# Optimization experiments

Measured on AMD Instinct MI355X. Metric: run time of the kernel, lower is better.

The kernel has to match this reference:

```python
import jax, jax.numpy as jnp
import numpy as np

N, E, G = 50000, 800000, 8
IN, ED = 128, 32


def gatv2_conv(x, src, dst, ea, Wl, bl, Wr, br, We, att, bias, n_nodes):
    """PyG GATv2Conv: add self loops (edge_attr fill='mean'), per-edge GATv2
    attention with leaky_relu(0.2), softmax over incoming edges per dst,
    scatter-add of alpha * x_l[src]; concat heads + bias."""
    H, C = att.shape
    e = src.shape[0]
    # self loops: edge attr = mean of incoming edge attrs per node (0 if none)
    loop = jnp.arange(n_nodes)
    cnt = jnp.maximum(jax.ops.segment_sum(jnp.ones((e,), x.dtype), dst, n_nodes), 1.0)
    ea_loop = jax.ops.segment_sum(ea, dst, n_nodes) / cnt[:, None]
    s = jnp.concatenate([src, loop])
    d = jnp.concatenate([dst, loop])
    ea_all = jnp.concatenate([ea, ea_loop], axis=0)
    xl = (x @ Wl + bl).reshape(n_nodes, H, C)
    xr = (x @ Wr + br).reshape(n_nodes, H, C)
    ee = (ea_all @ We).reshape(-1, H, C)
    m = jax.nn.leaky_relu(xl[s] + xr[d] + ee, 0.2)          # [Etot,H,C]
    alpha = jnp.einsum('ehc,hc->eh', m, att)                 # [Etot,H]
    amax = jax.ops.segment_max(alpha, d, n_nodes)            # every node has self loop
    p = jnp.exp(alpha - amax[d])
    denom = jax.ops.segment_sum(p, d, n_nodes)
    a = p / denom[d]                                         # [Etot,H]
    out = jax.ops.segment_sum(xl[s] * a[..., None], d, n_nodes)
    return out.reshape(n_nodes, H * C) + bias


def setup_inputs() -> dict:
    key = jax.random.key(0)
    ks = jax.random.split(key, 32)
    def gl(k, shape, fan):
        return jax.random.normal(k, shape, jnp.float32) / np.sqrt(fan)
    inp = {
        'x': jax.random.normal(ks[0], (N, IN), jnp.float32),
        'edge_index': jax.random.randint(ks[1], (2, E), 0, N),
        'edge_attr': jax.random.normal(ks[2], (E, ED), jnp.float32),
        'batch': jnp.sort(jax.random.randint(ks[3], (N,), 0, G)),
        # conv1: in=128 -> heads=2, out=64
        'Wl1': gl(ks[4], (IN, 128), IN), 'bl1': jnp.zeros((128,), jnp.float32),
        'Wr1': gl(ks[5], (IN, 128), IN), 'br1': jnp.zeros((128,), jnp.float32),
        'We1': gl(ks[6], (ED, 128), ED),
        'att1': gl(ks[7], (2, 64), 64), 'bias1': jnp.zeros((128,), jnp.float32),
        # conv2: in=128 -> heads=3, out=64
        'Wl2': gl(ks[8], (128, 192), 128), 'bl2': jnp.zeros((192,), jnp.float32),
        'Wr2': gl(ks[9], (128, 192), 128), 'br2': jnp.zeros((192,), jnp.float32),
        'We2': gl(ks[10], (ED, 192), ED),
        'att2': gl(ks[11], (3, 64), 64), 'bias2': jnp.zeros((192,), jnp.float32),
        # MLP head
        'W1': gl(ks[12], (192, 64), 192), 'c1': jnp.zeros((64,), jnp.float32),
        'W2': gl(ks[13], (64, 32), 64),  'c2': jnp.zeros((32,), jnp.float32),
        'W3': gl(ks[14], (32, 16), 32),  'c3': jnp.zeros((16,), jnp.float32),
        'W4': gl(ks[15], (16, 8), 16),   'c4': jnp.zeros((8,), jnp.float32),
        'W5': gl(ks[16], (8, 1), 8),     'c5': jnp.zeros((1,), jnp.float32),
        'W6': gl(ks[17], (1, 1), 1),     'c6': jnp.zeros((1,), jnp.float32),
    }
    return inp


def reference(x, edge_index, edge_attr, batch,
              Wl1, bl1, Wr1, br1, We1, att1, bias1,
              Wl2, bl2, Wr2, br2, We2, att2, bias2,
              W1, c1, W2, c2, W3, c3, W4, c4, W5, c5, W6, c6):
    lrelu = lambda t: jax.nn.leaky_relu(t, 0.01)  # nn.LeakyReLU default slope
    src, dst = edge_index[0], edge_index[1]
    h = lrelu(gatv2_conv(x, src, dst, edge_attr, Wl1, bl1, Wr1, br1, We1, att1, bias1, N))
    h = lrelu(gatv2_conv(h, src, dst, edge_attr, Wl2, bl2, Wr2, br2, We2, att2, bias2, N))
    g = jax.ops.segment_sum(h, batch, G)           # global_add_pool -> [G,192]
    g = lrelu(g @ W1 + c1)
    g = lrelu(g @ W2 + c2)
    g = lrelu(g @ W3 + c3)
    g = lrelu(g @ W4 + c4)
    g = g @ W5 + c5
    g = g @ W6 + c6
    return g
```

## Files before the change

kernel.cpp:

```cpp
#include <hip/hip_runtime.h>
#include <hip/hip_bf16.h>
#include <math.h>


typedef __attribute__((ext_vector_type(8))) short short8v;
typedef __attribute__((ext_vector_type(4))) float f32x4;

__device__ __forceinline__ unsigned short f2bf(float f) {
    union { float f; unsigned u; } v; v.f = f;
    unsigned r = v.u + 0x7fff + ((v.u >> 16) & 1);
    return (unsigned short)(r >> 16);
}
__device__ __forceinline__ float bf2f(unsigned short b) {
    union { unsigned u; float f; } v; v.u = ((unsigned)b) << 16;
    return v.f;
}

__device__ __forceinline__ int xcd_swizzle(int bid, int nwg) {
    int sq = nwg >> 3, sr = nwg & 7;
    int xcd = bid & 7, idx = bid >> 3;
    return (xcd < sr ? xcd * (sq + 1) : sr * (sq + 1) + (xcd - sr) * sq) + idx;
}

__global__ void k_deg(const int* __restrict__ dst, int E, int* __restrict__ deg) {
    int e = blockIdx.x * blockDim.x + threadIdx.x;
    if (e < E) atomicAdd(&deg[dst[e]], 1);
}

__global__ void k_scan1(const int* __restrict__ deg, int N,
                        int* __restrict__ incl, int* __restrict__ bsum) {
    __shared__ int ws4[4];
    const int tid = threadIdx.x;
    const int lane = tid & 63, w = tid >> 6;
    const int base = blockIdx.x * 2048;
    int v[8];
    int s = 0;
#pragma unroll
    for (int j = 0; j < 8; ++j) {
        int i = base + tid * 8 + j;
        v[j] = (i < N) ? deg[i] : 0;
        s += v[j];
    }
    int ps = s;
#pragma unroll
    for (int off = 1; off < 64; off <<= 1) {
        int t = __shfl_up(ps, off);
        if (lane >= off) ps += t;
    }
    if (lane == 63) ws4[w] = ps;
    __syncthreads();
    int woffs = 0;
#pragma unroll
    for (int k = 0; k < 4; ++k)
        if (k < w) woffs += ws4[k];
    int run = ps - s + woffs;
#pragma unroll
    for (int j = 0; j < 8; ++j) {
        run += v[j];
        int i = base + tid * 8 + j;
        if (i < N) incl[i] = run;
    }
    if (tid == 255) bsum[blockIdx.x] = run;
}

__global__ void k_scan2(int* __restrict__ bsum, int nb) {
    if (threadIdx.x == 0) {
        int c = 0;
        for (int k = 0; k < nb; ++k) { int t = bsum[k]; bsum[k] = c; c += t; }
    }
}

__global__ void k_scan3(const int* __restrict__ incl, const int* __restrict__ deg,
                        const int* __restrict__ boff, int N,
                        int* __restrict__ row_ptr, int* __restrict__ woff) {
    int i = blockIdx.x * blockDim.x + threadIdx.x;
    if (i < N) {
        int v = incl[i] + boff[i >> 11];
        row_ptr[i + 1] = v;
        woff[i] = v - deg[i];
        if (i == 0) row_ptr[0] = 0;
    }
}

__global__ void k_scatter(const int* __restrict__ src, const int* __restrict__ dst,
                          int E, int* __restrict__ woff, int* __restrict__ cidx,
                          int* __restrict__ s_csr, int* __restrict__ d_csr) {
    int e = blockIdx.x * blockDim.x + threadIdx.x;
    if (e < E) {
        int d = dst[e];
        int p = atomicAdd(&woff[d], 1);
        cidx[p] = e;
        s_csr[p] = src[e];
        d_csr[p] = d;
    }
}

__global__ void k_easeg(const float* __restrict__ ea, const int* __restrict__ cidx,
                        const int* __restrict__ row_ptr, int N,
                        float* __restrict__ easum) {
    const int t = blockIdx.x * blockDim.x + threadIdx.x;
    const int w = t >> 5;
    const int lane = threadIdx.x & 31;
    if (w >= N) return;
    const int beg = row_ptr[w], end = row_ptr[w + 1];
    float s = 0.f;
    for (int i = beg; i < end; ++i) {
        int e = cidx[i];
        s += ea[(size_t)e * 32 + lane];
    }
    easum[(size_t)w * 32 + lane] = s;
}

template <int HC>
__global__ __launch_bounds__(256, 2) void k_xw(
        const float* __restrict__ in, int N,
        const float* __restrict__ Wl, const float* __restrict__ bl,
        const float* __restrict__ Wr, const float* __restrict__ br,
        unsigned short* __restrict__ outl, unsigned short* __restrict__ outr) {
    __shared__ float Xs[128][68];
    __shared__ float Ws[128][64];
    const int tid = threadIdx.x;
    const int m0 = blockIdx.x * 64;
    const int cc = blockIdx.y;

#pragma unroll
    for (int t = 0; t < 8; ++t) {
        int idx4 = tid + t * 256;
        int r = idx4 >> 5, k4 = idx4 & 31;
        int n = m0 + r;
        float4 v = make_float4(0.f, 0.f, 0.f, 0.f);
        if (n < N) v = ((const float4*)in)[(size_t)n * 32 + k4];
        Xs[k4 * 4 + 0][r] = v.x;
        Xs[k4 * 4 + 1][r] = v.y;
        Xs[k4 * 4 + 2][r] = v.z;
        Xs[k4 * 4 + 3][r] = v.w;
    }

    const int rm = tid >> 4, rn = tid & 15;
    float acc[4][4];

#pragma unroll
    for (int mat = 0; mat < 2; ++mat) {
        const float* W = mat ? Wr : Wl;
        const float* b = mat ? br : bl;
        unsigned short* out = mat ? outr : outl;
        __syncthreads();
#pragma unroll
        for (int i = tid; i < 128 * 64; i += 256) {
            int k = i >> 6, c = i & 63;
            Ws[k][c] = W[(size_t)k * HC + cc * 64 + c];
        }
        __syncthreads();
#pragma unroll
        for (int i = 0; i < 4; ++i)
#pragma unroll
            for (int j = 0; j < 4; ++j) acc[i][j] = 0.f;
#pragma unroll 8
        for (int k = 0; k < 128; ++k) {
            float4 a = *(const float4*)&Xs[k][rm * 4];
            float4 bv = *(const float4*)&Ws[k][rn * 4];
            acc[0][0] += a.x * bv.x; acc[0][1] += a.x * bv.y;
            acc[0][2] += a.x * bv.z; acc[0][3] += a.x * bv.w;
            acc[1][0] += a.y * bv.x; acc[1][1] += a.y * bv.y;
            acc[1][2] += a.y * bv.z; acc[1][3] += a.y * bv.w;
            acc[2][0] += a.z * bv.x; acc[2][1] += a.z * bv.y;
            acc[2][2] += a.z * bv.z; acc[2][3] += a.z * bv.w;
            acc[3][0] += a.w * bv.x; acc[3][1] += a.w * bv.y;
            acc[3][2] += a.w * bv.z; acc[3][3] += a.w * bv.w;
        }
        float4 bb = *(const float4*)&b[cc * 64 + rn * 4];
#pragma unroll
        for (int i = 0; i < 4; ++i) {
            int n = m0 + rm * 4 + i;
            if (n < N) {
                ushort4 o;
                o.x = f2bf(acc[i][0] + bb.x);
                o.y = f2bf(acc[i][1] + bb.y);
                o.z = f2bf(acc[i][2] + bb.z);
                o.w = f2bf(acc[i][3] + bb.w);
                *(ushort4*)&out[(size_t)n * HC + cc * 64 + rn * 4] = o;
            }
        }
    }
}

template <int HC>
__global__ __launch_bounds__(256, 2) void k_ee(
        const float* __restrict__ A, int M,
        const float* __restrict__ We,
        float* __restrict__ out) {
    __shared__ float As[32][68];
    __shared__ float Ws[32][64];
    const int tid = threadIdx.x;
    const int m0 = blockIdx.x * 64;
    const int cc = blockIdx.y;

#pragma unroll
    for (int t = 0; t < 2; ++t) {
        int idx4 = tid + t * 256;
        int r = idx4 >> 3, q = idx4 & 7;
        int n = m0 + r;
        float4 v = make_float4(0.f, 0.f, 0.f, 0.f);
        if (n < M) v = ((const float4*)A)[(size_t)n * 8 + q];
        As[q * 4 + 0][r] = v.x;
        As[q * 4 + 1][r] = v.y;
        As[q * 4 + 2][r] = v.z;
        As[q * 4 + 3][r] = v.w;
    }
#pragma unroll
    for (int i = tid; i < 32 * 64; i += 256) {
        int k = i >> 6, c = i & 63;
        Ws[k][c] = We[(size_t)k * HC + cc * 64 + c];
    }
    __syncthreads();

    const int rm = tid >> 4, rn = tid & 15;
    float acc[4][4];
#pragma unroll
    for (int i = 0; i < 4; ++i)
#pragma unroll
        for (int j = 0; j < 4; ++j) acc[i][j] = 0.f;
#pragma unroll
    for (int k = 0; k < 32; ++k) {
        float4 a = *(const float4*)&As[k][rm * 4];
        float4 bv = *(const float4*)&Ws[k][rn * 4];
        acc[0][0] += a.x * bv.x; acc[0][1] += a.x * bv.y;
        acc[0][2] += a.x * bv.z; acc[0][3] += a.x * bv.w;
        acc[1][0] += a.y * bv.x; acc[1][1] += a.y * bv.y;
        acc[1][2] += a.y * bv.z; acc[1][3] += a.y * bv.w;
        acc[2][0] += a.z * bv.x; acc[2][1] += a.z * bv.y;
        acc[2][2] += a.z * bv.z; acc[2][3] += a.z * bv.w;
        acc[3][0] += a.w * bv.x; acc[3][1] += a.w * bv.y;
        acc[3][2] += a.w * bv.z; acc[3][3] += a.w * bv.w;
    }
#pragma unroll
    for (int i = 0; i < 4; ++i) {
        int n = m0 + rm * 4 + i;
        if (n < M) {
            float4 o = make_float4(acc[i][0], acc[i][1], acc[i][2], acc[i][3]);
            *(float4*)&out[(size_t)n * HC + cc * 64 + rn * 4] = o;
        }
    }
}

template <int H>
__global__ __launch_bounds__(256, 2) void k_fused(
        const unsigned short* __restrict__ xlb, const unsigned short* __restrict__ xrb,
        const float* __restrict__ ea,
        const int* __restrict__ cidx, const int* __restrict__ s_csr,
        const int* __restrict__ d_csr, int E,
        const float* __restrict__ We, const float* __restrict__ att,
        float* __restrict__ alpha) {
    constexpr int HC = H * 64;
    __shared__ __align__(16) unsigned short Wsb[HC][40];
    __shared__ int Es[64], Ss[64], Ds[64];
    const int tid = threadIdx.x;
    const int wg = xcd_swizzle(blockIdx.x, gridDim.x);
    const int i0 = wg * 64;

    if (tid < 64) {
        int i = i0 + tid;
        bool ok = i < E;
        Es[tid] = ok ? cidx[i] : 0;
        Ss[tid] = ok ? s_csr[i] : 0;
        Ds[tid] = ok ? d_csr[i] : 0;
    }
    for (int idx4 = tid; idx4 < 32 * (HC / 4); idx4 += 256) {
        int k = idx4 / (HC / 4), c4 = idx4 % (HC / 4);
        float4 v = ((const float4*)We)[idx4];
        Wsb[c4 * 4 + 0][k] = f2bf(v.x);
        Wsb[c4 * 4 + 1][k] = f2bf(v.y);
        Wsb[c4 * 4 + 2][k] = f2bf(v.z);
        Wsb[c4 * 4 + 3][k] = f2bf(v.w);
    }
    __syncthreads();

    const int lane = tid & 63;
    const int w = tid >> 6;
    const int lm = lane & 15;
    const int lk = lane >> 4;
    const int k0 = lk * 8;

    short8v afrag;
    {
        int eidx = Es[w * 16 + lm];
        const float4* ap = (const float4*)(ea + (size_t)eidx * 32 + k0);
        float4 v0 = ap[0], v1 = ap[1];
        afrag[0] = (short)f2bf(v0.x); afrag[1] = (short)f2bf(v0.y);
        afrag[2] = (short)f2bf(v0.z); afrag[3] = (short)f2bf(v0.w);
        afrag[4] = (short)f2bf(v1.x); afrag[5] = (short)f2bf(v1.y);
        afrag[6] = (short)f2bf(v1.z); afrag[7] = (short)f2bf(v1.w);
    }
    int sN[4], dN[4], gOk[4];
#pragma unroll
    for (int r = 0; r < 4; ++r) {
        int el = w * 16 + lk * 4 + r;
        sN[r] = Ss[el];
        dN[r] = Ds[el];
        gOk[r] = (i0 + el) < E;
    }

#pragma unroll
    for (int cc = 0; cc < H; ++cc) {
        float part[4] = {0.f, 0.f, 0.f, 0.f};
#pragma unroll
        for (int cg = 0; cg < 4; ++cg) {
            const int col = cc * 64 + cg * 16 + lm;
            short8v bfrag = *(const short8v*)&Wsb[col][k0];
            f32x4 dacc = {0.f, 0.f, 0.f, 0.f};
            dacc = __builtin_amdgcn_mfma_f32_16x16x32_bf16(afrag, bfrag, dacc, 0, 0, 0);
            float attv = att[col];
#pragma unroll
            for (int r = 0; r < 4; ++r) {
                float xa = bf2f(xlb[(size_t)sN[r] * HC + col]);
                float xb = bf2f(xrb[(size_t)dN[r] * HC + col]);
                float mv = xa + xb + dacc[r];
                mv = mv > 0.f ? mv : 0.2f * mv;
                part[r] += mv * attv;
            }
        }
#pragma unroll
        for (int off = 1; off < 16; off <<= 1)
#pragma unroll
            for (int r = 0; r < 4; ++r) part[r] += __shfl_xor(part[r], off);
        if (lm == 0) {
#pragma unroll
            for (int r = 0; r < 4; ++r) {
                if (gOk[r]) {
                    int gi = i0 + w * 16 + lk * 4 + r;
                    alpha[(size_t)gi * H + cc] = part[r];
                }
            }
        }
    }
}

template <int H, bool RELU>
__global__ __launch_bounds__(256, 2) void k_aggr(
        const unsigned short* __restrict__ xlb, const unsigned short* __restrict__ xrb,
        const float* __restrict__ EEself, const int* __restrict__ deg,
        const float* __restrict__ att,
        const int* __restrict__ s_csr, const int* __restrict__ row_ptr,
        const float* __restrict__ alpha,
        const float* __restrict__ bias, int Nn,
        float* __restrict__ out) {
    constexpr int HC = H * 64;
    const int lane = threadIdx.x & 63;
    const int wg = xcd_swizzle(blockIdx.x, gridDim.x);
    const int n = wg * 4 + ((int)threadIdx.x >> 6);
    if (n >= Nn) return;

    float m[H], den[H], acc[H];
    {
        int dg = deg[n];
        float inv = 1.f / (float)(dg > 0 ? dg : 1);
        float al[H];
#pragma unroll
        for (int h = 0; h < H; ++h) {
            float xlv = bf2f(xlb[(size_t)n * HC + h * 64 + lane]);
            float v = xlv + bf2f(xrb[(size_t)n * HC + h * 64 + lane])
                    + EEself[(size_t)n * HC + h * 64 + lane] * inv;
            v = v > 0.f ? v : 0.2f * v;
            al[h] = v * att[h * 64 + lane];
            acc[h] = xlv;
        }
#pragma unroll
        for (int off = 1; off < 64; off <<= 1)
#pragma unroll
            for (int h = 0; h < H; ++h) al[h] += __shfl_xor(al[h], off);
#pragma unroll
        for (int h = 0; h < H; ++h) { m[h] = al[h]; den[h] = 1.f; }
    }

    const int beg = row_ptr[n], end = row_ptr[n + 1];
    int i = beg;
    for (; i + 3 < end; i += 4) {
        int s0 = s_csr[i], s1 = s_csr[i + 1], s2 = s_csr[i + 2], s3 = s_csr[i + 3];
        float a0[H], a1[H], a2[H], a3[H], xv0[H], xv1[H], xv2[H], xv3[H];
#pragma unroll
        for (int h = 0; h < H; ++h) {
            a0[h] = alpha[(size_t)i * H + h];
            a1[h] = alpha[(size_t)(i + 1) * H + h];
            a2[h] = alpha[(size_t)(i + 2) * H + h];
            a3[h] = alpha[(size_t)(i + 3) * H + h];
            xv0[h] = bf2f(xlb[(size_t)s0 * HC + h * 64 + lane]);
            xv1[h] = bf2f(xlb[(size_t)s1 * HC + h * 64 + lane]);
            xv2[h] = bf2f(xlb[(size_t)s2 * HC + h * 64 + lane]);
            xv3[h] = bf2f(xlb[(size_t)s3 * HC + h * 64 + lane]);
        }
#pragma unroll
        for (int h = 0; h < H; ++h) {
            float mx01 = fmaxf(a0[h], a1[h]);
            float mx23 = fmaxf(a2[h], a3[h]);
            float nm = fmaxf(m[h], fmaxf(mx01, mx23));
            float corr = __expf(m[h] - nm);
            float p0 = __expf(a0[h] - nm);
            float p1 = __expf(a1[h] - nm);
            float p2 = __expf(a2[h] - nm);
            float p3 = __expf(a3[h] - nm);
            den[h] = den[h] * corr + (p0 + p1) + (p2 + p3);
            acc[h] = acc[h] * corr + (p0 * xv0[h] + p1 * xv1[h])
                                   + (p2 * xv2[h] + p3 * xv3[h]);
            m[h] = nm;
        }
    }
    for (; i < end; ++i) {
        int s = s_csr[i];
#pragma unroll
        for (int h = 0; h < H; ++h) {
            float a = alpha[(size_t)i * H + h];
            float xv = bf2f(xlb[(size_t)s * HC + h * 64 + lane]);
            float nm = fmaxf(m[h], a);
            float corr = __expf(m[h] - nm);
            float p = __expf(a - nm);
            den[h] = den[h] * corr + p;
            acc[h] = acc[h] * corr + p * xv;
            m[h] = nm;
        }
    }
#pragma unroll
    for (int h = 0; h < H; ++h) {
        float r = acc[h] / den[h] + bias[h * 64 + lane];
        if (RELU) r = r > 0.f ? r : 0.01f * r;
        out[(size_t)n * HC + h * 64 + lane] = r;
    }
}

__global__ void k_pool(const float* __restrict__ h2, const int* __restrict__ batch,
                       int Nn, float* __restrict__ g) {
    const int c = threadIdx.x;
    const int n0 = blockIdx.x * 128;
    if (n0 >= Nn) return;
    const int n1 = (n0 + 128 < Nn) ? n0 + 128 : Nn;
    float s = 0.f;
    int cur = batch[n0];
    for (int n = n0; n < n1; ++n) {
        int b = batch[n];
        if (b != cur) {
            atomicAdd(&g[cur * 192 + c], s);
            s = 0.f;
            cur = b;
        }
        s += h2[(size_t)n * 192 + c];
    }
    atomicAdd(&g[cur * 192 + c], s);
}

__global__ void k_mlp(const float* __restrict__ g,
                      const float* W1, const float* c1, const float* W2, const float* c2,
                      const float* W3, const float* c3, const float* W4, const float* c4,
                      const float* W5, const float* c5, const float* W6, const float* c6,
                      float* __restrict__ out) {
    __shared__ float t0[8 * 192];
    __shared__ float t1[8 * 64];
    __shared__ float t2[8 * 32];
    __shared__ float t3[8 * 16];
    __shared__ float t4[8 * 8];
    const int tid = threadIdx.x;
    for (int i = tid; i < 8 * 192; i += 256) t0[i] = g[i];
    __syncthreads();
    for (int i = tid; i < 8 * 64; i += 256) {
        int r = i >> 6, c = i & 63;
        float s = c1[c];
        for (int k = 0; k < 192; ++k) s += t0[r * 192 + k] * W1[k * 64 + c];
        t1[i] = s > 0.f ? s : 0.01f * s;
    }
    __syncthreads();
    for (int i = tid; i < 8 * 32; i += 256) {
        int r = i >> 5, c = i & 31;
        float s = c2[c];
        for (int k = 0; k < 64; ++k) s += t1[r * 64 + k] * W2[k * 32 + c];
        t2[i] = s > 0.f ? s : 0.01f * s;
    }
    __syncthreads();
    for (int i = tid; i < 8 * 16; i += 256) {
        int r = i >> 4, c = i & 15;
        float s = c3[c];
        for (int k = 0; k < 32; ++k) s += t2[r * 32 + k] * W3[k * 16 + c];
        t3[i] = s > 0.f ? s : 0.01f * s;
    }
    __syncthreads();
    for (int i = tid; i < 8 * 8; i += 256) {
        int r = i >> 3, c = i & 7;
        float s = c4[c];
        for (int k = 0; k < 16; ++k) s += t3[r * 16 + k] * W4[k * 8 + c];
        t4[i] = s > 0.f ? s : 0.01f * s;
    }
    __syncthreads();
    if (tid < 8) {
        float s = c5[0];
        for (int k = 0; k < 8; ++k) s += t4[tid * 8 + k] * W5[k];
        s = s * W6[0] + c6[0];
        out[tid] = s;
    }
}

extern "C" void kernel_launch(void* const* d_in, const int* in_sizes, int n_in,
                              void* d_out, int out_size, void* d_ws, size_t ws_size,
                              hipStream_t stream) {
    const float* x     = (const float*)d_in[0];
    const int*   eidx  = (const int*)d_in[1];
    const float* ea    = (const float*)d_in[2];
    const int*   batch = (const int*)d_in[3];
    const float* Wl1 = (const float*)d_in[4];
    const float* bl1 = (const float*)d_in[5];
    const float* Wr1 = (const float*)d_in[6];
    const float* br1 = (const float*)d_in[7];
    const float* We1 = (const float*)d_in[8];
    const float* att1 = (const float*)d_in[9];
    const float* bias1 = (const float*)d_in[10];
    const float* Wl2 = (const float*)d_in[11];
    const float* bl2 = (const float*)d_in[12];
    const float* Wr2 = (const float*)d_in[13];
    const float* br2 = (const float*)d_in[14];
    const float* We2 = (const float*)d_in[15];
    const float* att2 = (const float*)d_in[16];
    const float* bias2 = (const float*)d_in[17];
    const float* W1 = (const float*)d_in[18];
    const float* c1 = (const float*)d_in[19];
    const float* W2 = (const float*)d_in[20];
    const float* c2 = (const float*)d_in[21];
    const float* W3 = (const float*)d_in[22];
    const float* c3 = (const float*)d_in[23];
    const float* W4 = (const float*)d_in[24];
    const float* c4 = (const float*)d_in[25];
    const float* W5 = (const float*)d_in[26];
    const float* c5 = (const float*)d_in[27];
    const float* W6 = (const float*)d_in[28];
    const float* c6 = (const float*)d_in[29];

    const int N = in_sizes[0] / 128;
    const int E = in_sizes[1] / 2;
    const int* srcs = eidx;
    const int* dsts = eidx + E;

    char* p = (char*)d_ws;
    auto alloc = [&](size_t bytes) -> char* {
        char* r = p;
        p += (bytes + 255) & ~(size_t)255;
        return r;
    };
    int*            deg     = (int*)alloc((size_t)N * 4);
    int*            row_ptr = (int*)alloc((size_t)(N + 1) * 4);
    int*            woff    = (int*)alloc((size_t)N * 4);
    int*            cidx    = (int*)alloc((size_t)E * 4);
    int*            s_csr   = (int*)alloc((size_t)E * 4);
    int*            d_csr   = (int*)alloc((size_t)E * 4);
    int*            incl    = (int*)alloc((size_t)N * 4);
    int*            bsum    = (int*)alloc(64 * 4);
    float*          easum   = (float*)alloc((size_t)N * 32 * 4);
    float*          EEself  = (float*)alloc((size_t)N * 192 * 4);
    unsigned short* xlb     = (unsigned short*)alloc((size_t)N * 192 * 2);
    unsigned short* xrb     = (unsigned short*)alloc((size_t)N * 192 * 2);
    float*          h1      = (float*)alloc((size_t)N * 128 * 4);
    float*          h2      = (float*)alloc((size_t)N * 192 * 4);
    float*          alpha   = (float*)alloc((size_t)E * 3 * 4);
    float*          gp      = (float*)alloc(8 * 192 * 4);

    hipMemsetAsync(deg, 0, (size_t)N * 4, stream);
    hipMemsetAsync(gp, 0, 8 * 192 * 4, stream);

    const int nb = (N + 2047) / 2048;
    k_deg<<<(E + 255) / 256, 256, 0, stream>>>(dsts, E, deg);
    k_scan1<<<nb, 256, 0, stream>>>(deg, N, incl, bsum);
    k_scan2<<<1, 64, 0, stream>>>(bsum, nb);
    k_scan3<<<(N + 255) / 256, 256, 0, stream>>>(incl, deg, bsum, N, row_ptr, woff);
    k_scatter<<<(E + 255) / 256, 256, 0, stream>>>(srcs, dsts, E, woff, cidx, s_csr, d_csr);

    const int mt = (N + 63) / 64;
    const int et = (E + 63) / 64;
    const int nblk = (N + 3) / 4;

    k_easeg<<<(N * 32 + 255) / 256, 256, 0, stream>>>(ea, cidx, row_ptr, N, easum);

    k_xw<128><<<dim3(mt, 2), 256, 0, stream>>>(x, N, Wl1, bl1, Wr1, br1, xlb, xrb);
    k_ee<128><<<dim3(mt, 2), 256, 0, stream>>>(easum, N, We1, EEself);
    k_fused<2><<<et, 256, 0, stream>>>(xlb, xrb, ea, cidx, s_csr, d_csr, E, We1, att1, alpha);
    k_aggr<2, true><<<nblk, 256, 0, stream>>>(xlb, xrb, EEself, deg, att1, s_csr, row_ptr,
                                              alpha, bias1, N, h1);

    k_xw<192><<<dim3(mt, 3), 256, 0, stream>>>(h1, N, Wl2, bl2, Wr2, br2, xlb, xrb);
    k_ee<192><<<dim3(mt, 3), 256, 0, stream>>>(easum, N, We2, EEself);
    k_fused<3><<<et, 256, 0, stream>>>(xlb, xrb, ea, cidx, s_csr, d_csr, E, We2, att2, alpha);
    k_aggr<3, true><<<nblk, 256, 0, stream>>>(xlb, xrb, EEself, deg, att2, s_csr, row_ptr,
                                              alpha, bias2, N, h2);

    k_pool<<<(N + 127) / 128, 192, 0, stream>>>(h2, batch, N, gp);
    k_mlp<<<1, 256, 0, stream>>>(gp, W1, c1, W2, c2, W3, c3, W4, c4, W5, c5, W6, c6,
                                 (float*)d_out);
}
```

Baseline: 801.5 us.

## Transpose MFMA operands in edge attention kernel to vectorize gathers and cut shuffles

Swaps the roles of the edge-attribute fragment and the We fragment in the 16x16x32 MFMA, so each output row now holds features and each column an edge. Each lane then owns a single edge with 4 consecutive feature columns. That allows ushort4/float4 vector gathers of xl, xr and att, where the old code issued scalar strided loads. The reduction across features shrinks from 4 shuffle rounds over 4 partials to 2 shuffles of one value. The We LDS layout is changed to a k-blocked form so the new A fragment loads contiguously.

```diff
diff --git a/kernel.cpp b/kernel.cpp
--- a/kernel.cpp
+++ b/kernel.cpp
@@ -252,7 +252,7 @@
         const float* __restrict__ We, const float* __restrict__ att,
         float* __restrict__ alpha) {
     constexpr int HC = H * 64;
-    __shared__ __align__(16) unsigned short Wsb[HC][40];
+    __shared__ __align__(16) unsigned short Wsb[4 * HC * 8];
     __shared__ int Es[64], Ss[64], Ds[64];
     const int tid = threadIdx.x;
     const int wg = xcd_swizzle(blockIdx.x, gridDim.x);
@@ -268,10 +268,11 @@
     for (int idx4 = tid; idx4 < 32 * (HC / 4); idx4 += 256) {
         int k = idx4 / (HC / 4), c4 = idx4 % (HC / 4);
         float4 v = ((const float4*)We)[idx4];
-        Wsb[c4 * 4 + 0][k] = f2bf(v.x);
-        Wsb[c4 * 4 + 1][k] = f2bf(v.y);
-        Wsb[c4 * 4 + 2][k] = f2bf(v.z);
-        Wsb[c4 * 4 + 3][k] = f2bf(v.w);
+        int base = (k >> 3) * HC * 8 + (k & 7);
+        Wsb[base + (c4 * 4 + 0) * 8] = f2bf(v.x);
+        Wsb[base + (c4 * 4 + 1) * 8] = f2bf(v.y);
+        Wsb[base + (c4 * 4 + 2) * 8] = f2bf(v.z);
+        Wsb[base + (c4 * 4 + 3) * 8] = f2bf(v.w);
     }
     __syncthreads();
 
@@ -281,57 +282,47 @@
     const int lk = lane >> 4;
     const int k0 = lk * 8;
 
-    short8v afrag;
+    const int el = w * 16 + lm;
+    const int eidx = Es[el];
+    const int sN = Ss[el], dN = Ds[el];
+    const bool ok = (i0 + el) < E;
+
+    short8v bfrag;
     {
-        int eidx = Es[w * 16 + lm];
-        const float4* ap = (const float4*)(ea + (size_t)eidx * 32 + k0);
-        float4 v0 = ap[0], v1 = ap[1];
-        afrag[0] = (short)f2bf(v0.x); afrag[1] = (short)f2bf(v0.y);
-        afrag[2] = (short)f2bf(v0.z); afrag[3] = (short)f2bf(v0.w);
-        afrag[4] = (short)f2bf(v1.x); afrag[5] = (short)f2bf(v1.y);
-        afrag[6] = (short)f2bf(v1.z); afrag[7] = (short)f2bf(v1.w);
-    }
-    int sN[4], dN[4], gOk[4];
-#pragma unroll
-    for (int r = 0; r < 4; ++r) {
-        int el = w * 16 + lk * 4 + r;
-        sN[r] = Ss[el];
-        dN[r] = Ds[el];
-        gOk[r] = (i0 + el) < E;
+        const float4* bp = (const float4*)(ea + (size_t)eidx * 32 + k0);
+        float4 v0 = bp[0], v1 = bp[1];
+        bfrag[0] = (short)f2bf(v0.x); bfrag[1] = (short)f2bf(v0.y);
+        bfrag[2] = (short)f2bf(v0.z); bfrag[3] = (short)f2bf(v0.w);
+        bfrag[4] = (short)f2bf(v1.x); bfrag[5] = (short)f2bf(v1.y);
+        bfrag[6] = (short)f2bf(v1.z); bfrag[7] = (short)f2bf(v1.w);
     }
 
 #pragma unroll
     for (int cc = 0; cc < H; ++cc) {
-        float part[4] = {0.f, 0.f, 0.f, 0.f};
+        float part = 0.f;
 #pragma unroll
         for (int cg = 0; cg < 4; ++cg) {
-            const int col = cc * 64 + cg * 16 + lm;
-            short8v bfrag = *(const short8v*)&Wsb[col][k0];
+            const int acol = cc * 64 + cg * 16 + lm;
+            short8v afrag = *(const short8v*)&Wsb[((size_t)lk * HC + acol) * 8];
             f32x4 dacc = {0.f, 0.f, 0.f, 0.f};
             dacc = __builtin_amdgcn_mfma_f32_16x16x32_bf16(afrag, bfrag, dacc, 0, 0, 0);
-            float attv = att[col];
-#pragma unroll
-            for (int r = 0; r < 4; ++r) {
-                float xa = bf2f(xlb[(size_t)sN[r] * HC + col]);
-                float xb = bf2f(xrb[(size_t)dN[r] * HC + col]);
-                float mv = xa + xb + dacc[r];
-                mv = mv > 0.f ? mv : 0.2f * mv;
-                part[r] += mv * attv;
-            }
-        }
-#pragma unroll
-        for (int off = 1; off < 16; off <<= 1)
-#pragma unroll
-            for (int r = 0; r < 4; ++r) part[r] += __shfl_xor(part[r], off);
-        if (lm == 0) {
-#pragma unroll
-            for (int r = 0; r < 4; ++r) {
-                if (gOk[r]) {
-                    int gi = i0 + w * 16 + lk * 4 + r;
-                    alpha[(size_t)gi * H + cc] = part[r];
-                }
-            }
-        }
+            const int col0 = cc * 64 + cg * 16 + lk * 4;
+            ushort4 xa = *(const ushort4*)&xlb[(size_t)sN * HC + col0];
+            ushort4 xb = *(const ushort4*)&xrb[(size_t)dN * HC + col0];
+            float4 at4 = *(const float4*)&att[col0];
+            float m0 = bf2f(xa.x) + bf2f(xb.x) + dacc[0];
+            float m1 = bf2f(xa.y) + bf2f(xb.y) + dacc[1];
+            float m2 = bf2f(xa.z) + bf2f(xb.z) + dacc[2];
+            float m3 = bf2f(xa.w) + bf2f(xb.w) + dacc[3];
+            m0 = m0 > 0.f ? m0 : 0.2f * m0;
+            m1 = m1 > 0.f ? m1 : 0.2f * m1;
+            m2 = m2 > 0.f ? m2 : 0.2f * m2;
+            m3 = m3 > 0.f ? m3 : 0.2f * m3;
+            part += m0 * at4.x + m1 * at4.y + m2 * at4.z + m3 * at4.w;
+        }
+        part += __shfl_xor(part, 16);
+        part += __shfl_xor(part, 32);
+        if (lk == 0 && ok) alpha[(size_t)(i0 + el) * H + cc] = part;
     }
 }
 
```

After: 811.6 us. No clear change (+1.3%).

## Use bf16 MFMA for node linear projections in k_xw

Applied to the files above, without the earlier changes.

Replaces the FP32 scalar-FMA tiled GEMM in k_xw with bf16 MFMA 16x16x32 instructions. A fragments are loaded straight from global memory into registers and converted to bf16, and W is staged transposed in shared memory as bf16. This aims to cut the compute and LDS cost of the x@Wl and x@Wr projections. In exchange the inputs are rounded to bf16 before the multiply, and the output stores become scalar 2-byte writes.

```diff
diff --git a/kernel.cpp b/kernel.cpp
--- a/kernel.cpp
+++ b/kernel.cpp
@@ -117,27 +117,28 @@
         const float* __restrict__ Wl, const float* __restrict__ bl,
         const float* __restrict__ Wr, const float* __restrict__ br,
         unsigned short* __restrict__ outl, unsigned short* __restrict__ outr) {
-    __shared__ float Xs[128][68];
-    __shared__ float Ws[128][64];
+    __shared__ __align__(16) unsigned short Wsb[64][136];
     const int tid = threadIdx.x;
     const int m0 = blockIdx.x * 64;
-    const int cc = blockIdx.y;
-
-#pragma unroll
-    for (int t = 0; t < 8; ++t) {
-        int idx4 = tid + t * 256;
-        int r = idx4 >> 5, k4 = idx4 & 31;
-        int n = m0 + r;
-        float4 v = make_float4(0.f, 0.f, 0.f, 0.f);
-        if (n < N) v = ((const float4*)in)[(size_t)n * 32 + k4];
-        Xs[k4 * 4 + 0][r] = v.x;
-        Xs[k4 * 4 + 1][r] = v.y;
-        Xs[k4 * 4 + 2][r] = v.z;
-        Xs[k4 * 4 + 3][r] = v.w;
-    }
-
-    const int rm = tid >> 4, rn = tid & 15;
-    float acc[4][4];
+    const int cc0 = blockIdx.y * 64;
+
+    const int lane = tid & 63;
+    const int w = tid >> 6;
+    const int lm = lane & 15;
+    const int lk = lane >> 4;
+
+    int node_in = m0 + w * 16 + lm;
+    if (node_in >= N) node_in = N - 1;
+    short8v afrag[4];
+#pragma unroll
+    for (int kc = 0; kc < 4; ++kc) {
+        const float4* ap = (const float4*)(in + (size_t)node_in * 128 + kc * 32 + lk * 8);
+        float4 v0 = ap[0], v1 = ap[1];
+        afrag[kc][0] = (short)f2bf(v0.x); afrag[kc][1] = (short)f2bf(v0.y);
+        afrag[kc][2] = (short)f2bf(v0.z); afrag[kc][3] = (short)f2bf(v0.w);
+        afrag[kc][4] = (short)f2bf(v1.x); afrag[kc][5] = (short)f2bf(v1.y);
+        afrag[kc][6] = (short)f2bf(v1.z); afrag[kc][7] = (short)f2bf(v1.w);
+    }
 
 #pragma unroll
     for (int mat = 0; mat < 2; ++mat) {
@@ -145,40 +146,30 @@
         const float* b = mat ? br : bl;
         unsigned short* out = mat ? outr : outl;
         __syncthreads();
-#pragma unroll
-        for (int i = tid; i < 128 * 64; i += 256) {
-            int k = i >> 6, c = i & 63;
-            Ws[k][c] = W[(size_t)k * HC + cc * 64 + c];
+        for (int i4 = tid; i4 < 128 * 16; i4 += 256) {
+            int k = i4 >> 4, c4 = i4 & 15;
+            float4 v = *(const float4*)&W[(size_t)k * HC + cc0 + c4 * 4];
+            Wsb[c4 * 4 + 0][k] = f2bf(v.x);
+            Wsb[c4 * 4 + 1][k] = f2bf(v.y);
+            Wsb[c4 * 4 + 2][k] = f2bf(v.z);
+            Wsb[c4 * 4 + 3][k] = f2bf(v.w);
         }
         __syncthreads();
-#pragma unroll
-        for (int i = 0; i < 4; ++i)
-#pragma unroll
-            for (int j = 0; j < 4; ++j) acc[i][j] = 0.f;
-#pragma unroll 8
-        for (int k = 0; k < 128; ++k) {
-            float4 a = *(const float4*)&Xs[k][rm * 4];
-            float4 bv = *(const float4*)&Ws[k][rn * 4];
-            acc[0][0] += a.x * bv.x; acc[0][1] += a.x * bv.y;
-            acc[0][2] += a.x * bv.z; acc[0][3] += a.x * bv.w;
-            acc[1][0] += a.y * bv.x; acc[1][1] += a.y * bv.y;
-            acc[1][2] += a.y * bv.z; acc[1][3] += a.y * bv.w;
-            acc[2][0] += a.z * bv.x; acc[2][1] += a.z * bv.y;
-            acc[2][2] += a.z * bv.z; acc[2][3] += a.z * bv.w;
-            acc[3][0] += a.w * bv.x; acc[3][1] += a.w * bv.y;
-            acc[3][2] += a.w * bv.z; acc[3][3] += a.w * bv.w;
-        }
-        float4 bb = *(const float4*)&b[cc * 64 + rn * 4];
-#pragma unroll
-        for (int i = 0; i < 4; ++i) {
-            int n = m0 + rm * 4 + i;
-            if (n < N) {
-                ushort4 o;
-                o.x = f2bf(acc[i][0] + bb.x);
-                o.y = f2bf(acc[i][1] + bb.y);
-                o.z = f2bf(acc[i][2] + bb.z);
-                o.w = f2bf(acc[i][3] + bb.w);
-                *(ushort4*)&out[(size_t)n * HC + cc * 64 + rn * 4] = o;
+
+#pragma unroll
+        for (int cg = 0; cg < 4; ++cg) {
+            f32x4 acc = {0.f, 0.f, 0.f, 0.f};
+#pragma unroll
+            for (int kc = 0; kc < 4; ++kc) {
+                short8v bfrag = *(const short8v*)&Wsb[cg * 16 + lm][kc * 32 + lk * 8];
+                acc = __builtin_amdgcn_mfma_f32_16x16x32_bf16(afrag[kc], bfrag, acc, 0, 0, 0);
+            }
+            const int col = cc0 + cg * 16 + lm;
+            const float bb = b[col];
+#pragma unroll
+            for (int r = 0; r < 4; ++r) {
+                int n = m0 + w * 16 + lk * 4 + r;
+                if (n < N) out[(size_t)n * HC + col] = f2bf(acc[r] + bb);
             }
         }
     }
```

After: 714.3 us. 10.9% less time.
